# Performance work log

Hardware: AMD Instinct MI355X
Metric: run time of the kernel (lower is better)

The kernel has to match this reference:

```python
import jax, jax.numpy as jnp
import numpy as np

HEADS = 8
DIM_HEAD = 64
ROPE_THETA = 10000.0


def _rope(t):
    # t: [b, h, n, d]; interleaved-pair rotation as in rotary-embedding-torch
    n, d = t.shape[-2], t.shape[-1]
    inv_freq = 1.0 / (ROPE_THETA ** (jnp.arange(0, d, 2, dtype=jnp.float32) / d))  # [d/2]
    freqs = jnp.arange(n, dtype=jnp.float32)[:, None] * inv_freq[None, :]  # [n, d/2]
    freqs = jnp.repeat(freqs, 2, axis=-1)  # [n, d], repeated per pair
    cos, sin = jnp.cos(freqs), jnp.sin(freqs)
    x1 = t[..., 0::2]
    x2 = t[..., 1::2]
    rot = jnp.stack((-x2, x1), axis=-1).reshape(t.shape)  # rotate_half
    return t * cos + rot * sin


def setup_inputs() -> dict:
    key = jax.random.key(0)
    k1, k2, k3, k4 = jax.random.split(key, 4)
    b, n, dim = 2, 2048, 512
    hidden = HEADS * DIM_HEAD
    x = jax.random.normal(k1, (b, n, dim), dtype=jnp.float32)
    pos_bias = jax.random.normal(k2, (HEADS, n, n), dtype=jnp.float32) * 0.02
    w_qkv = jax.random.normal(k3, (dim, 3 * hidden), dtype=jnp.float32) * (dim ** -0.5)
    w_out = jax.random.normal(k4, (hidden, dim), dtype=jnp.float32) * (hidden ** -0.5)
    return {"x": x, "pos_bias": pos_bias, "w_qkv": w_qkv, "w_out": w_out}


def reference(x, pos_bias, w_qkv, w_out):
    b, n, _ = x.shape
    qkv = x @ w_qkv  # [b, n, 3*hidden]
    q, k, v = jnp.split(qkv, 3, axis=-1)

    def to_heads(t):
        return t.reshape(b, n, HEADS, DIM_HEAD).transpose(0, 2, 1, 3)  # [b,h,n,d]

    q, k, v = map(to_heads, (q, k, v))
    k = _rope(k)
    q = _rope(q * (DIM_HEAD ** -0.5))
    sim = jnp.einsum('bhid,bhjd->bhij', q, k)  # [b,h,n,n]
    sim = sim + pos_bias  # broadcast over batch
    sim = sim - jax.lax.stop_gradient(jnp.max(sim, axis=-1, keepdims=True))
    attn = jax.nn.softmax(sim, axis=-1)
    out = jnp.einsum('bhij,bhjd->bhid', attn, v)
    out = out.transpose(0, 2, 1, 3).reshape(b, n, HEADS * DIM_HEAD)
    return out @ w_out
```

## Files before the change

kernel.cpp:

```cpp
#include <hip/hip_runtime.h>
#include <math.h>

#define SEQ 2048
#define NHEAD 8
#define HDIM 64
#define BATCH 2

typedef __attribute__((ext_vector_type(8))) short short8;
typedef __attribute__((ext_vector_type(4))) float f32x4;

__device__ __forceinline__ ushort f2bf(float f) {
    union { float f; unsigned u; } v; v.f = f;
    unsigned r = v.u + 0x7FFFu + ((v.u >> 16) & 1u);
    return (ushort)(r >> 16);
}

__device__ __forceinline__ f32x4 mfma16(short8 a, short8 b, f32x4 c) {
    return __builtin_amdgcn_mfma_f32_16x16x32_bf16(a, b, c, 0, 0, 0);
}

__global__ __launch_bounds__(256)
void pack_x(const float* __restrict__ x, ushort* __restrict__ xb)
{
    const int i = (blockIdx.x * 256 + threadIdx.x) * 8;
    float4 a = *(const float4*)&x[i];
    float4 b = *(const float4*)&x[i + 4];
    union { ushort us[8]; uint4 v; } pk;
    pk.us[0] = f2bf(a.x); pk.us[1] = f2bf(a.y); pk.us[2] = f2bf(a.z); pk.us[3] = f2bf(a.w);
    pk.us[4] = f2bf(b.x); pk.us[5] = f2bf(b.y); pk.us[6] = f2bf(b.z); pk.us[7] = f2bf(b.w);
    *(uint4*)&xb[i] = pk.v;
}

__global__ __launch_bounds__(256)
void transpose_w(const float* __restrict__ w, ushort* __restrict__ wT, int K, int N)
{
    __shared__ ushort tile[64][66];
    const int t = threadIdx.x;
    const int n0 = blockIdx.x * 64, k0 = blockIdx.y * 64;
#pragma unroll
    for (int i = 0; i < 4; ++i) {
        const int slot = t + i * 256;
        const int r = slot >> 4, c4 = (slot & 15) * 4;
        float4 v = *(const float4*)&w[(size_t)(k0 + r) * N + n0 + c4];
        tile[c4 + 0][r] = f2bf(v.x);
        tile[c4 + 1][r] = f2bf(v.y);
        tile[c4 + 2][r] = f2bf(v.z);
        tile[c4 + 3][r] = f2bf(v.w);
    }
    __syncthreads();
    const int n = t >> 2, kc = (t & 3) * 16;
    union { ushort us[16]; uint4 v[2]; } o;
#pragma unroll
    for (int j = 0; j < 16; ++j) o.us[j] = tile[n][kc + j];
    *(uint4*)&wT[(size_t)(n0 + n) * K + k0 + kc]     = o.v[0];
    *(uint4*)&wT[(size_t)(n0 + n) * K + k0 + kc + 8] = o.v[1];
}

__global__ __launch_bounds__(256)
void gemm_qkv_rope(const ushort* __restrict__ xb, const ushort* __restrict__ wT,
                   ushort* __restrict__ qb, ushort* __restrict__ kb,
                   ushort* __restrict__ vtb)
{
    __shared__ __align__(16) ushort As[128][72];
    __shared__ __align__(16) ushort Bs[128][72];
    const int t = threadIdx.x, lane = t & 63, w = t >> 6;
    const int quad = lane >> 4, l16 = lane & 15;
    const int m0 = blockIdx.y * 128, n0 = blockIdx.x * 128;
    const int mw = (w >> 1) * 64, nw = (w & 1) * 64;
    f32x4 acc[4][4] = {};

    for (int k0 = 0; k0 < 512; k0 += 64) {
#pragma unroll
        for (int i = 0; i < 4; ++i) {
            const int slot = t + i * 256;
            const int r = slot >> 3, sg = (slot & 7) * 8;
            *(uint4*)&As[r][sg] = *(const uint4*)&xb[(size_t)(m0 + r) * 512 + k0 + sg];
            *(uint4*)&Bs[r][sg] = *(const uint4*)&wT[(size_t)(n0 + r) * 512 + k0 + sg];
        }
        __syncthreads();
#pragma unroll
        for (int ks = 0; ks < 2; ++ks) {
            short8 a[4], b[4];
#pragma unroll
            for (int i = 0; i < 4; ++i)
                a[i] = *(const short8*)&As[mw + i * 16 + l16][ks * 32 + quad * 8];
#pragma unroll
            for (int j = 0; j < 4; ++j)
                b[j] = *(const short8*)&Bs[nw + j * 16 + l16][ks * 32 + quad * 8];
#pragma unroll
            for (int i = 0; i < 4; ++i)
#pragma unroll
                for (int j = 0; j < 4; ++j)
                    acc[i][j] = mfma16(a[i], b[j], acc[i][j]);
        }
        __syncthreads();
    }

    const int sec = (n0 + nw) >> 9;
    if (sec == 2) {
#pragma unroll
        for (int i = 0; i < 4; ++i) {
            const int m = m0 + mw + i * 16 + quad * 4;
            const int bidx = m >> 11, n = m & 2047;
#pragma unroll
            for (int j = 0; j < 4; ++j) {
                const int nc = n0 + nw + j * 16 + l16;
                const int d = nc & 63, h = (nc >> 6) & 7;
                ushort4 pk;
                pk.x = f2bf(acc[i][j][0]); pk.y = f2bf(acc[i][j][1]);
                pk.z = f2bf(acc[i][j][2]); pk.w = f2bf(acc[i][j][3]);
                *(ushort4*)&vtb[(((size_t)bidx * 8 + h) * 64 + d) * 2048 + n] = pk;
            }
        }
    } else {
        ushort* dst = (sec == 0) ? qb : kb;
        const float scale = (sec == 0) ? 0.125f : 1.0f;
#pragma unroll
        for (int j = 0; j < 4; ++j) {
            const int nc = n0 + nw + j * 16 + l16;
            const int d = nc & 63, h = (nc >> 6) & 7;
            const float inv = __expf(-(float)(d & ~1) * (9.2103403719761836f / 64.0f));
#pragma unroll
            for (int i = 0; i < 4; ++i)
#pragma unroll
            for (int r = 0; r < 4; ++r) {
                const int m = m0 + mw + i * 16 + quad * 4 + r;
                const int bidx = m >> 11, n = m & 2047;
                float sn, cs;
                __sincosf((float)n * inv, &sn, &cs);
                const float vacc = acc[i][j][r];
                const float partner = __shfl_xor(vacc, 1);
                const float rot = (d & 1) ? (vacc * cs + partner * sn)
                                          : (vacc * cs - partner * sn);
                dst[(((size_t)bidx * 8 + h) * 2048 + n) * 64 + d] = f2bf(rot * scale);
            }
        }
    }
}

__global__ __launch_bounds__(256)
void flash_attn_mfma(const ushort* __restrict__ qb, const ushort* __restrict__ kb,
                     const ushort* __restrict__ vtb, const float* __restrict__ bias,
                     ushort* __restrict__ ob)
{
    __shared__ __align__(16) ushort Ks[64][72];
    __shared__ __align__(16) ushort Vt[64][72];
    __shared__ __align__(16) ushort Ps[4][16][72];
    const int t = threadIdx.x, lane = t & 63, w = t >> 6;
    const int quad = lane >> 4, l16 = lane & 15;
    const int q0 = blockIdx.x * 64, h = blockIdx.y, b = blockIdx.z;
    const size_t bh = (size_t)(b * NHEAD + h);
    const ushort* Q  = qb  + bh * SEQ * HDIM;
    const ushort* K  = kb  + bh * SEQ * HDIM;
    const ushort* VT = vtb + bh * HDIM * SEQ;

    short8 qf[2];
    qf[0] = *(const short8*)&Q[(size_t)(q0 + w * 16 + l16) * HDIM + quad * 8];
    qf[1] = *(const short8*)&Q[(size_t)(q0 + w * 16 + l16) * HDIM + 32 + quad * 8];

    f32x4 oacc[4] = {};
    float lsum[4] = {};
    const float* bias_base = bias + ((size_t)h * SEQ + q0 + w * 16 + quad * 4) * SEQ;

    for (int k0 = 0; k0 < SEQ; k0 += 64) {
        float bv[4][4];
#pragma unroll
        for (int r = 0; r < 4; ++r)
#pragma unroll
            for (int s = 0; s < 4; ++s)
                bv[r][s] = bias_base[(size_t)r * SEQ + k0 + s * 16 + l16];

#pragma unroll
        for (int i = 0; i < 2; ++i) {
            const int slot = t + i * 256;
            const int r = slot >> 3, sg = (slot & 7) * 8;
            *(uint4*)&Ks[r][sg] = *(const uint4*)&K[(size_t)(k0 + r) * HDIM + sg];
            *(uint4*)&Vt[r][sg] = *(const uint4*)&VT[(size_t)r * SEQ + k0 + sg];
        }
        __syncthreads();

        f32x4 sacc[4] = {};
#pragma unroll
        for (int ks = 0; ks < 2; ++ks)
#pragma unroll
            for (int s = 0; s < 4; ++s) {
                short8 kf = *(const short8*)&Ks[s * 16 + l16][ks * 32 + quad * 8];
                sacc[s] = mfma16(qf[ks], kf, sacc[s]);
            }

#pragma unroll
        for (int r = 0; r < 4; ++r) {
#pragma unroll
            for (int s = 0; s < 4; ++s) {
                const float p = __expf(sacc[s][r] + bv[r][s]);
                lsum[r] += p;
                Ps[w][quad * 4 + r][s * 16 + l16] = f2bf(p);
            }
        }
        asm volatile("" ::: "memory");

#pragma unroll
        for (int ks = 0; ks < 2; ++ks) {
            short8 pf = *(const short8*)&Ps[w][l16][ks * 32 + quad * 8];
#pragma unroll
            for (int s = 0; s < 4; ++s) {
                short8 vf = *(const short8*)&Vt[s * 16 + l16][ks * 32 + quad * 8];
                oacc[s] = mfma16(pf, vf, oacc[s]);
            }
        }
        __syncthreads();
    }

#pragma unroll
    for (int r = 0; r < 4; ++r) {
        float rs = lsum[r];
        rs += __shfl_xor(rs, 1, 16);
        rs += __shfl_xor(rs, 2, 16);
        rs += __shfl_xor(rs, 4, 16);
        rs += __shfl_xor(rs, 8, 16);
        const float invl = 1.0f / rs;
        const size_t m = (size_t)b * SEQ + q0 + w * 16 + quad * 4 + r;
#pragma unroll
        for (int s = 0; s < 4; ++s)
            ob[m * 512 + h * HDIM + s * 16 + l16] = f2bf(oacc[s][r] * invl);
    }
}

__global__ __launch_bounds__(256)
void gemm_out(const ushort* __restrict__ Ab, const ushort* __restrict__ wT,
              float* __restrict__ C)
{
    __shared__ __align__(16) ushort As[64][72];
    __shared__ __align__(16) ushort Bs[128][72];
    const int t = threadIdx.x, lane = t & 63, w = t >> 6;
    const int quad = lane >> 4, l16 = lane & 15;
    const int m0 = blockIdx.y * 64, n0 = blockIdx.x * 128;
    const int mw = (w >> 1) * 32, nw = (w & 1) * 64;
    f32x4 acc[2][4] = {};

    for (int k0 = 0; k0 < 512; k0 += 64) {
#pragma unroll
        for (int i = 0; i < 2; ++i) {
            const int slot = t + i * 256;
            const int r = slot >> 3, sg = (slot & 7) * 8;
            *(uint4*)&As[r][sg] = *(const uint4*)&Ab[(size_t)(m0 + r) * 512 + k0 + sg];
        }
#pragma unroll
        for (int i = 0; i < 4; ++i) {
            const int slot = t + i * 256;
            const int r = slot >> 3, sg = (slot & 7) * 8;
            *(uint4*)&Bs[r][sg] = *(const uint4*)&wT[(size_t)(n0 + r) * 512 + k0 + sg];
        }
        __syncthreads();
#pragma unroll
        for (int ks = 0; ks < 2; ++ks) {
            short8 a[2], b[4];
#pragma unroll
            for (int i = 0; i < 2; ++i)
                a[i] = *(const short8*)&As[mw + i * 16 + l16][ks * 32 + quad * 8];
#pragma unroll
            for (int j = 0; j < 4; ++j)
                b[j] = *(const short8*)&Bs[nw + j * 16 + l16][ks * 32 + quad * 8];
#pragma unroll
            for (int i = 0; i < 2; ++i)
#pragma unroll
                for (int j = 0; j < 4; ++j)
                    acc[i][j] = mfma16(a[i], b[j], acc[i][j]);
        }
        __syncthreads();
    }
#pragma unroll
    for (int i = 0; i < 2; ++i)
#pragma unroll
    for (int r = 0; r < 4; ++r) {
        const int m = m0 + mw + i * 16 + quad * 4 + r;
#pragma unroll
        for (int j = 0; j < 4; ++j)
            C[(size_t)m * 512 + n0 + nw + j * 16 + l16] = acc[i][j][r];
    }
}

extern "C" void kernel_launch(void* const* d_in, const int* in_sizes, int n_in,
                              void* d_out, int out_size, void* d_ws, size_t ws_size,
                              hipStream_t stream)
{
    const float* x        = (const float*)d_in[0];
    const float* pos_bias = (const float*)d_in[1];
    const float* w_qkv    = (const float*)d_in[2];
    const float* w_out    = (const float*)d_in[3];
    float* out = (float*)d_out;

    char* ws = (char*)d_ws;
    ushort* xb     = (ushort*)(ws);
    ushort* wqkvT  = (ushort*)(ws + 4194304);
    ushort* woutT  = (ushort*)(ws + 5767168);
    ushort* qb     = (ushort*)(ws + 6291456);
    ushort* kb     = (ushort*)(ws + 10485760);
    ushort* vtb    = (ushort*)(ws + 14680064);
    ushort* attnb  = (ushort*)(ws + 18874368);

    pack_x<<<1024, 256, 0, stream>>>(x, xb);
    transpose_w<<<dim3(24, 8), 256, 0, stream>>>(w_qkv, wqkvT, 512, 1536);
    transpose_w<<<dim3(8, 8), 256, 0, stream>>>(w_out, woutT, 512, 512);
    gemm_qkv_rope<<<dim3(12, 32), 256, 0, stream>>>(xb, wqkvT, qb, kb, vtb);
    flash_attn_mfma<<<dim3(SEQ / 64, NHEAD, BATCH), 256, 0, stream>>>(qb, kb, vtb, pos_bias, attnb);
    gemm_out<<<dim3(4, 64), 256, 0, stream>>>(attnb, woutT, out);
}
```

Measured before the change: 285.3 us.

## Split attention over key chunks, prefetch tiles, merge prep kernels, shrink GEMM tiles

Merges the x-pack and the two weight transposes into one launch. The attention kernel is split four ways along the key axis, with a new combine kernel that sums the partial outputs and row sums, which raises the grid from 512 to 2048 blocks. K, V and bias tiles are now register-prefetched one step ahead, and the two GEMMs use smaller tiles with register prefetch to get more blocks per GPU. The split adds fp32 partial-output traffic through workspace and an extra launch. Combining partials without any max rescaling is still exact, because the original kernel also did not subtract a running max.

```diff
diff --git a/kernel.cpp b/kernel.cpp
--- a/kernel.cpp
+++ b/kernel.cpp
@@ -20,23 +20,25 @@
 }
 
 __global__ __launch_bounds__(256)
-void pack_x(const float* __restrict__ x, ushort* __restrict__ xb)
-{
-    const int i = (blockIdx.x * 256 + threadIdx.x) * 8;
-    float4 a = *(const float4*)&x[i];
-    float4 b = *(const float4*)&x[i + 4];
-    union { ushort us[8]; uint4 v; } pk;
-    pk.us[0] = f2bf(a.x); pk.us[1] = f2bf(a.y); pk.us[2] = f2bf(a.z); pk.us[3] = f2bf(a.w);
-    pk.us[4] = f2bf(b.x); pk.us[5] = f2bf(b.y); pk.us[6] = f2bf(b.z); pk.us[7] = f2bf(b.w);
-    *(uint4*)&xb[i] = pk.v;
-}
-
-__global__ __launch_bounds__(256)
-void transpose_w(const float* __restrict__ w, ushort* __restrict__ wT, int K, int N)
+void prep(const float* __restrict__ x, const float* __restrict__ w_qkv,
+          const float* __restrict__ w_out, ushort* __restrict__ xb,
+          ushort* __restrict__ wqkvT, ushort* __restrict__ woutT)
 {
     __shared__ ushort tile[64][66];
-    const int t = threadIdx.x;
-    const int n0 = blockIdx.x * 64, k0 = blockIdx.y * 64;
+    const int blk = blockIdx.x, t = threadIdx.x;
+    if (blk < 1024) {
+        const int i = (blk * 256 + t) * 8;
+        float4 a = *(const float4*)&x[i];
+        float4 b = *(const float4*)&x[i + 4];
+        union { ushort us[8]; uint4 v; } pk;
+        pk.us[0] = f2bf(a.x); pk.us[1] = f2bf(a.y); pk.us[2] = f2bf(a.z); pk.us[3] = f2bf(a.w);
+        pk.us[4] = f2bf(b.x); pk.us[5] = f2bf(b.y); pk.us[6] = f2bf(b.z); pk.us[7] = f2bf(b.w);
+        *(uint4*)&xb[i] = pk.v;
+        return;
+    }
+    const float* w; ushort* wT; int K, N, n0, k0;
+    if (blk < 1216) { const int s = blk - 1024; w = w_qkv; wT = wqkvT; K = 512; N = 1536; n0 = (s % 24) * 64; k0 = (s / 24) * 64; }
+    else            { const int s = blk - 1216; w = w_out; wT = woutT; K = 512; N = 512;  n0 = (s % 8) * 64;  k0 = (s / 8) * 64; }
 #pragma unroll
     for (int i = 0; i < 4; ++i) {
         const int slot = t + i * 256;
@@ -61,34 +63,48 @@
                    ushort* __restrict__ qb, ushort* __restrict__ kb,
                    ushort* __restrict__ vtb)
 {
-    __shared__ __align__(16) ushort As[128][72];
+    __shared__ __align__(16) ushort As[64][72];
     __shared__ __align__(16) ushort Bs[128][72];
     const int t = threadIdx.x, lane = t & 63, w = t >> 6;
     const int quad = lane >> 4, l16 = lane & 15;
-    const int m0 = blockIdx.y * 128, n0 = blockIdx.x * 128;
-    const int mw = (w >> 1) * 64, nw = (w & 1) * 64;
-    f32x4 acc[4][4] = {};
+    const int m0 = blockIdx.y * 64, n0 = blockIdx.x * 128;
+    const int mw = (w >> 1) * 32, nw = (w & 1) * 64;
+    f32x4 acc[2][4] = {};
+
+    const int ra = t >> 3, sg = (t & 7) * 8;
+    uint4 ar[2], br[4];
+#pragma unroll
+    for (int i = 0; i < 2; ++i)
+        ar[i] = *(const uint4*)&xb[(size_t)(m0 + ra + i * 32) * 512 + sg];
+#pragma unroll
+    for (int i = 0; i < 4; ++i)
+        br[i] = *(const uint4*)&wT[(size_t)(n0 + ra + i * 32) * 512 + sg];
 
     for (int k0 = 0; k0 < 512; k0 += 64) {
 #pragma unroll
-        for (int i = 0; i < 4; ++i) {
-            const int slot = t + i * 256;
-            const int r = slot >> 3, sg = (slot & 7) * 8;
-            *(uint4*)&As[r][sg] = *(const uint4*)&xb[(size_t)(m0 + r) * 512 + k0 + sg];
-            *(uint4*)&Bs[r][sg] = *(const uint4*)&wT[(size_t)(n0 + r) * 512 + k0 + sg];
-        }
-        __syncthreads();
+        for (int i = 0; i < 2; ++i) *(uint4*)&As[ra + i * 32][sg] = ar[i];
+#pragma unroll
+        for (int i = 0; i < 4; ++i) *(uint4*)&Bs[ra + i * 32][sg] = br[i];
+        __syncthreads();
+        if (k0 < 448) {
+#pragma unroll
+            for (int i = 0; i < 2; ++i)
+                ar[i] = *(const uint4*)&xb[(size_t)(m0 + ra + i * 32) * 512 + k0 + 64 + sg];
+#pragma unroll
+            for (int i = 0; i < 4; ++i)
+                br[i] = *(const uint4*)&wT[(size_t)(n0 + ra + i * 32) * 512 + k0 + 64 + sg];
+        }
 #pragma unroll
         for (int ks = 0; ks < 2; ++ks) {
-            short8 a[4], b[4];
-#pragma unroll
-            for (int i = 0; i < 4; ++i)
+            short8 a[2], b[4];
+#pragma unroll
+            for (int i = 0; i < 2; ++i)
                 a[i] = *(const short8*)&As[mw + i * 16 + l16][ks * 32 + quad * 8];
 #pragma unroll
             for (int j = 0; j < 4; ++j)
                 b[j] = *(const short8*)&Bs[nw + j * 16 + l16][ks * 32 + quad * 8];
 #pragma unroll
-            for (int i = 0; i < 4; ++i)
+            for (int i = 0; i < 2; ++i)
 #pragma unroll
                 for (int j = 0; j < 4; ++j)
                     acc[i][j] = mfma16(a[i], b[j], acc[i][j]);
@@ -99,7 +115,7 @@
     const int sec = (n0 + nw) >> 9;
     if (sec == 2) {
 #pragma unroll
-        for (int i = 0; i < 4; ++i) {
+        for (int i = 0; i < 2; ++i) {
             const int m = m0 + mw + i * 16 + quad * 4;
             const int bidx = m >> 11, n = m & 2047;
 #pragma unroll
@@ -121,7 +137,7 @@
             const int d = nc & 63, h = (nc >> 6) & 7;
             const float inv = __expf(-(float)(d & ~1) * (9.2103403719761836f / 64.0f));
 #pragma unroll
-            for (int i = 0; i < 4; ++i)
+            for (int i = 0; i < 2; ++i)
 #pragma unroll
             for (int r = 0; r < 4; ++r) {
                 const int m = m0 + mw + i * 16 + quad * 4 + r;
@@ -139,16 +155,18 @@
 }
 
 __global__ __launch_bounds__(256)
-void flash_attn_mfma(const ushort* __restrict__ qb, const ushort* __restrict__ kb,
-                     const ushort* __restrict__ vtb, const float* __restrict__ bias,
-                     ushort* __restrict__ ob)
+void flash_attn_split(const ushort* __restrict__ qb, const ushort* __restrict__ kb,
+                      const ushort* __restrict__ vtb, const float* __restrict__ bias,
+                      float* __restrict__ opart, float* __restrict__ lsump)
 {
     __shared__ __align__(16) ushort Ks[64][72];
     __shared__ __align__(16) ushort Vt[64][72];
     __shared__ __align__(16) ushort Ps[4][16][72];
     const int t = threadIdx.x, lane = t & 63, w = t >> 6;
     const int quad = lane >> 4, l16 = lane & 15;
-    const int q0 = blockIdx.x * 64, h = blockIdx.y, b = blockIdx.z;
+    const int q0 = blockIdx.x * 64, h = blockIdx.y;
+    const int b = blockIdx.z >> 2, split = blockIdx.z & 3;
+    const int kbase = split * 512;
     const size_t bh = (size_t)(b * NHEAD + h);
     const ushort* Q  = qb  + bh * SEQ * HDIM;
     const ushort* K  = kb  + bh * SEQ * HDIM;
@@ -162,22 +180,43 @@
     float lsum[4] = {};
     const float* bias_base = bias + ((size_t)h * SEQ + q0 + w * 16 + quad * 4) * SEQ;
 
-    for (int k0 = 0; k0 < SEQ; k0 += 64) {
-        float bv[4][4];
-#pragma unroll
-        for (int r = 0; r < 4; ++r)
-#pragma unroll
-            for (int s = 0; s < 4; ++s)
-                bv[r][s] = bias_base[(size_t)r * SEQ + k0 + s * 16 + l16];
-
+    const int ra = t >> 3, sg = (t & 7) * 8;
+    uint4 kr[2], vr[2];
+#pragma unroll
+    for (int i = 0; i < 2; ++i) {
+        kr[i] = *(const uint4*)&K[(size_t)(kbase + ra + i * 32) * HDIM + sg];
+        vr[i] = *(const uint4*)&VT[(size_t)(ra + i * 32) * SEQ + kbase + sg];
+    }
+    float bv[4][4];
+#pragma unroll
+    for (int r = 0; r < 4; ++r)
+#pragma unroll
+        for (int s = 0; s < 4; ++s)
+            bv[r][s] = bias_base[(size_t)r * SEQ + kbase + s * 16 + l16];
+
+#pragma unroll
+    for (int it = 0; it < 8; ++it) {
+        const int k0 = kbase + it * 64;
 #pragma unroll
         for (int i = 0; i < 2; ++i) {
-            const int slot = t + i * 256;
-            const int r = slot >> 3, sg = (slot & 7) * 8;
-            *(uint4*)&Ks[r][sg] = *(const uint4*)&K[(size_t)(k0 + r) * HDIM + sg];
-            *(uint4*)&Vt[r][sg] = *(const uint4*)&VT[(size_t)r * SEQ + k0 + sg];
-        }
-        __syncthreads();
+            *(uint4*)&Ks[ra + i * 32][sg] = kr[i];
+            *(uint4*)&Vt[ra + i * 32][sg] = vr[i];
+        }
+        __syncthreads();
+
+        float bvn[4][4];
+        if (it < 7) {
+#pragma unroll
+            for (int i = 0; i < 2; ++i) {
+                kr[i] = *(const uint4*)&K[(size_t)(k0 + 64 + ra + i * 32) * HDIM + sg];
+                vr[i] = *(const uint4*)&VT[(size_t)(ra + i * 32) * SEQ + k0 + 64 + sg];
+            }
+#pragma unroll
+            for (int r = 0; r < 4; ++r)
+#pragma unroll
+                for (int s = 0; s < 4; ++s)
+                    bvn[r][s] = bias_base[(size_t)r * SEQ + k0 + 64 + s * 16 + l16];
+        }
 
         f32x4 sacc[4] = {};
 #pragma unroll
@@ -189,14 +228,13 @@
             }
 
 #pragma unroll
-        for (int r = 0; r < 4; ++r) {
+        for (int r = 0; r < 4; ++r)
 #pragma unroll
             for (int s = 0; s < 4; ++s) {
                 const float p = __expf(sacc[s][r] + bv[r][s]);
                 lsum[r] += p;
                 Ps[w][quad * 4 + r][s * 16 + l16] = f2bf(p);
             }
-        }
         asm volatile("" ::: "memory");
 
 #pragma unroll
@@ -209,21 +247,53 @@
             }
         }
         __syncthreads();
-    }
-
+
+        if (it < 7) {
+#pragma unroll
+            for (int r = 0; r < 4; ++r)
+#pragma unroll
+                for (int s = 0; s < 4; ++s) bv[r][s] = bvn[r][s];
+        }
+    }
+
+    const size_t pbase = ((size_t)bh * 4 + split) * SEQ;
 #pragma unroll
     for (int r = 0; r < 4; ++r) {
+        const int row = q0 + w * 16 + quad * 4 + r;
         float rs = lsum[r];
         rs += __shfl_xor(rs, 1, 16);
         rs += __shfl_xor(rs, 2, 16);
         rs += __shfl_xor(rs, 4, 16);
         rs += __shfl_xor(rs, 8, 16);
-        const float invl = 1.0f / rs;
-        const size_t m = (size_t)b * SEQ + q0 + w * 16 + quad * 4 + r;
 #pragma unroll
         for (int s = 0; s < 4; ++s)
-            ob[m * 512 + h * HDIM + s * 16 + l16] = f2bf(oacc[s][r] * invl);
-    }
+            opart[(pbase + row) * 64 + s * 16 + l16] = oacc[s][r];
+        if (l16 == 0) lsump[pbase + row] = rs;
+    }
+}
+
+__global__ __launch_bounds__(256)
+void combine(const float* __restrict__ opart, const float* __restrict__ lsump,
+             ushort* __restrict__ attnb)
+{
+    const int tid = blockIdx.x * 256 + threadIdx.x;
+    const int d4 = (tid & 15) * 4;
+    const int n  = (tid >> 4) & 2047;
+    const int bh = tid >> 15;
+    float ox = 0, oy = 0, oz = 0, ow = 0, L = 0;
+#pragma unroll
+    for (int s = 0; s < 4; ++s) {
+        const size_t base = ((size_t)bh * 4 + s) * SEQ + n;
+        float4 p = *(const float4*)&opart[base * 64 + d4];
+        ox += p.x; oy += p.y; oz += p.z; ow += p.w;
+        L += lsump[base];
+    }
+    const float inv = 1.0f / L;
+    ushort4 pk;
+    pk.x = f2bf(ox * inv); pk.y = f2bf(oy * inv);
+    pk.z = f2bf(oz * inv); pk.w = f2bf(ow * inv);
+    const int b = bh >> 3, h = bh & 7;
+    *(ushort4*)&attnb[((size_t)b * SEQ + n) * 512 + h * 64 + d4] = pk;
 }
 
 __global__ __launch_bounds__(256)
@@ -231,40 +301,48 @@
               float* __restrict__ C)
 {
     __shared__ __align__(16) ushort As[64][72];
-    __shared__ __align__(16) ushort Bs[128][72];
+    __shared__ __align__(16) ushort Bs[64][72];
     const int t = threadIdx.x, lane = t & 63, w = t >> 6;
     const int quad = lane >> 4, l16 = lane & 15;
-    const int m0 = blockIdx.y * 64, n0 = blockIdx.x * 128;
-    const int mw = (w >> 1) * 32, nw = (w & 1) * 64;
-    f32x4 acc[2][4] = {};
+    const int m0 = blockIdx.y * 64, n0 = blockIdx.x * 64;
+    const int mw = (w >> 1) * 32, nw = (w & 1) * 32;
+    f32x4 acc[2][2] = {};
+
+    const int ra = t >> 3, sg = (t & 7) * 8;
+    uint4 ar[2], br[2];
+#pragma unroll
+    for (int i = 0; i < 2; ++i) {
+        ar[i] = *(const uint4*)&Ab[(size_t)(m0 + ra + i * 32) * 512 + sg];
+        br[i] = *(const uint4*)&wT[(size_t)(n0 + ra + i * 32) * 512 + sg];
+    }
 
     for (int k0 = 0; k0 < 512; k0 += 64) {
 #pragma unroll
         for (int i = 0; i < 2; ++i) {
-            const int slot = t + i * 256;
-            const int r = slot >> 3, sg = (slot & 7) * 8;
-            *(uint4*)&As[r][sg] = *(const uint4*)&Ab[(size_t)(m0 + r) * 512 + k0 + sg];
-        }
-#pragma unroll
-        for (int i = 0; i < 4; ++i) {
-            const int slot = t + i * 256;
-            const int r = slot >> 3, sg = (slot & 7) * 8;
-            *(uint4*)&Bs[r][sg] = *(const uint4*)&wT[(size_t)(n0 + r) * 512 + k0 + sg];
-        }
-        __syncthreads();
+            *(uint4*)&As[ra + i * 32][sg] = ar[i];
+            *(uint4*)&Bs[ra + i * 32][sg] = br[i];
+        }
+        __syncthreads();
+        if (k0 < 448) {
+#pragma unroll
+            for (int i = 0; i < 2; ++i) {
+                ar[i] = *(const uint4*)&Ab[(size_t)(m0 + ra + i * 32) * 512 + k0 + 64 + sg];
+                br[i] = *(const uint4*)&wT[(size_t)(n0 + ra + i * 32) * 512 + k0 + 64 + sg];
+            }
+        }
 #pragma unroll
         for (int ks = 0; ks < 2; ++ks) {
-            short8 a[2], b[4];
+            short8 a[2], b[2];
 #pragma unroll
             for (int i = 0; i < 2; ++i)
                 a[i] = *(const short8*)&As[mw + i * 16 + l16][ks * 32 + quad * 8];
 #pragma unroll
-            for (int j = 0; j < 4; ++j)
+            for (int j = 0; j < 2; ++j)
                 b[j] = *(const short8*)&Bs[nw + j * 16 + l16][ks * 32 + quad * 8];
 #pragma unroll
             for (int i = 0; i < 2; ++i)
 #pragma unroll
-                for (int j = 0; j < 4; ++j)
+                for (int j = 0; j < 2; ++j)
                     acc[i][j] = mfma16(a[i], b[j], acc[i][j]);
         }
         __syncthreads();
@@ -275,7 +353,7 @@
     for (int r = 0; r < 4; ++r) {
         const int m = m0 + mw + i * 16 + quad * 4 + r;
 #pragma unroll
-        for (int j = 0; j < 4; ++j)
+        for (int j = 0; j < 2; ++j)
             C[(size_t)m * 512 + n0 + nw + j * 16 + l16] = acc[i][j][r];
     }
 }
@@ -298,11 +376,12 @@
     ushort* kb     = (ushort*)(ws + 10485760);
     ushort* vtb    = (ushort*)(ws + 14680064);
     ushort* attnb  = (ushort*)(ws + 18874368);
-
-    pack_x<<<1024, 256, 0, stream>>>(x, xb);
-    transpose_w<<<dim3(24, 8), 256, 0, stream>>>(w_qkv, wqkvT, 512, 1536);
-    transpose_w<<<dim3(8, 8), 256, 0, stream>>>(w_out, woutT, 512, 512);
-    gemm_qkv_rope<<<dim3(12, 32), 256, 0, stream>>>(xb, wqkvT, qb, kb, vtb);
-    flash_attn_mfma<<<dim3(SEQ / 64, NHEAD, BATCH), 256, 0, stream>>>(qb, kb, vtb, pos_bias, attnb);
-    gemm_out<<<dim3(4, 64), 256, 0, stream>>>(attnb, woutT, out);
-}
+    float*  opart  = (float*) (ws + 23068672);
+    float*  lsump  = (float*) (ws + 56623104);
+
+    prep<<<1280, 256, 0, stream>>>(x, w_qkv, w_out, xb, wqkvT, woutT);
+    gemm_qkv_rope<<<dim3(12, 64), 256, 0, stream>>>(xb, wqkvT, qb, kb, vtb);
+    flash_attn_split<<<dim3(SEQ / 64, NHEAD, BATCH * 4), 256, 0, stream>>>(qb, kb, vtb, pos_bias, opart, lsump);
+    combine<<<2048, 256, 0, stream>>>(opart, lsump, attnb);
+    gemm_out<<<dim3(8, 64), 256, 0, stream>>>(attnb, woutT, out);
+}
```

After: 353.8 us. 24.0% more time.

## Merge prep kernels and switch GEMMs and attention to single-wave register-fed blocks

Applied to the files above, without the earlier changes.

Folds the three preprocessing kernels into one launch. Rewrites both GEMMs and the attention kernel as one-wavefront blocks that load MFMA operands straight from global memory instead of staging them through shared memory with block barriers. Attention now double-buffers K, V and bias fragments in registers to overlap loads with compute. This removes LDS traffic and syncs, at the cost of losing operand reuse across waves (more global/L2 traffic) and higher register pressure.

```diff
diff --git a/kernel.cpp b/kernel.cpp
--- a/kernel.cpp
+++ b/kernel.cpp
@@ -20,23 +20,25 @@
 }
 
 __global__ __launch_bounds__(256)
-void pack_x(const float* __restrict__ x, ushort* __restrict__ xb)
-{
-    const int i = (blockIdx.x * 256 + threadIdx.x) * 8;
-    float4 a = *(const float4*)&x[i];
-    float4 b = *(const float4*)&x[i + 4];
-    union { ushort us[8]; uint4 v; } pk;
-    pk.us[0] = f2bf(a.x); pk.us[1] = f2bf(a.y); pk.us[2] = f2bf(a.z); pk.us[3] = f2bf(a.w);
-    pk.us[4] = f2bf(b.x); pk.us[5] = f2bf(b.y); pk.us[6] = f2bf(b.z); pk.us[7] = f2bf(b.w);
-    *(uint4*)&xb[i] = pk.v;
-}
-
-__global__ __launch_bounds__(256)
-void transpose_w(const float* __restrict__ w, ushort* __restrict__ wT, int K, int N)
+void prep(const float* __restrict__ x, const float* __restrict__ w_qkv,
+          const float* __restrict__ w_out, ushort* __restrict__ xb,
+          ushort* __restrict__ wqkvT, ushort* __restrict__ woutT)
 {
     __shared__ ushort tile[64][66];
-    const int t = threadIdx.x;
-    const int n0 = blockIdx.x * 64, k0 = blockIdx.y * 64;
+    const int blk = blockIdx.x, t = threadIdx.x;
+    if (blk < 1024) {
+        const int i = (blk * 256 + t) * 8;
+        float4 a = *(const float4*)&x[i];
+        float4 b = *(const float4*)&x[i + 4];
+        union { ushort us[8]; uint4 v; } pk;
+        pk.us[0] = f2bf(a.x); pk.us[1] = f2bf(a.y); pk.us[2] = f2bf(a.z); pk.us[3] = f2bf(a.w);
+        pk.us[4] = f2bf(b.x); pk.us[5] = f2bf(b.y); pk.us[6] = f2bf(b.z); pk.us[7] = f2bf(b.w);
+        *(uint4*)&xb[i] = pk.v;
+        return;
+    }
+    const float* w; ushort* wT; int K, N, n0, k0;
+    if (blk < 1216) { const int s = blk - 1024; w = w_qkv; wT = wqkvT; K = 512; N = 1536; n0 = (s % 24) * 64; k0 = (s / 24) * 64; }
+    else            { const int s = blk - 1216; w = w_out; wT = woutT; K = 512; N = 512;  n0 = (s % 8) * 64;  k0 = (s / 8) * 64; }
 #pragma unroll
     for (int i = 0; i < 4; ++i) {
         const int slot = t + i * 256;
@@ -56,56 +58,40 @@
     *(uint4*)&wT[(size_t)(n0 + n) * K + k0 + kc + 8] = o.v[1];
 }
 
-__global__ __launch_bounds__(256)
+__global__ __launch_bounds__(64)
 void gemm_qkv_rope(const ushort* __restrict__ xb, const ushort* __restrict__ wT,
                    ushort* __restrict__ qb, ushort* __restrict__ kb,
                    ushort* __restrict__ vtb)
 {
-    __shared__ __align__(16) ushort As[128][72];
-    __shared__ __align__(16) ushort Bs[128][72];
-    const int t = threadIdx.x, lane = t & 63, w = t >> 6;
-    const int quad = lane >> 4, l16 = lane & 15;
-    const int m0 = blockIdx.y * 128, n0 = blockIdx.x * 128;
-    const int mw = (w >> 1) * 64, nw = (w & 1) * 64;
-    f32x4 acc[4][4] = {};
-
-    for (int k0 = 0; k0 < 512; k0 += 64) {
-#pragma unroll
-        for (int i = 0; i < 4; ++i) {
-            const int slot = t + i * 256;
-            const int r = slot >> 3, sg = (slot & 7) * 8;
-            *(uint4*)&As[r][sg] = *(const uint4*)&xb[(size_t)(m0 + r) * 512 + k0 + sg];
-            *(uint4*)&Bs[r][sg] = *(const uint4*)&wT[(size_t)(n0 + r) * 512 + k0 + sg];
-        }
-        __syncthreads();
-#pragma unroll
-        for (int ks = 0; ks < 2; ++ks) {
-            short8 a[4], b[4];
-#pragma unroll
-            for (int i = 0; i < 4; ++i)
-                a[i] = *(const short8*)&As[mw + i * 16 + l16][ks * 32 + quad * 8];
+    const int lane = threadIdx.x, quad = lane >> 4, l16 = lane & 15;
+    const int n0 = blockIdx.x * 64, m0 = blockIdx.y * 32;
+    f32x4 acc[2][4] = {};
+
+#pragma unroll 4
+    for (int k0 = 0; k0 < 512; k0 += 32) {
+        short8 a[2], bfr[4];
+#pragma unroll
+        for (int i = 0; i < 2; ++i)
+            a[i] = *(const short8*)&xb[(size_t)(m0 + i * 16 + l16) * 512 + k0 + quad * 8];
+#pragma unroll
+        for (int j = 0; j < 4; ++j)
+            bfr[j] = *(const short8*)&wT[(size_t)(n0 + j * 16 + l16) * 512 + k0 + quad * 8];
+#pragma unroll
+        for (int i = 0; i < 2; ++i)
 #pragma unroll
             for (int j = 0; j < 4; ++j)
-                b[j] = *(const short8*)&Bs[nw + j * 16 + l16][ks * 32 + quad * 8];
-#pragma unroll
-            for (int i = 0; i < 4; ++i)
-#pragma unroll
-                for (int j = 0; j < 4; ++j)
-                    acc[i][j] = mfma16(a[i], b[j], acc[i][j]);
-        }
-        __syncthreads();
-    }
-
-    const int sec = (n0 + nw) >> 9;
+                acc[i][j] = mfma16(a[i], bfr[j], acc[i][j]);
+    }
+
+    const int sec = n0 >> 9;
     if (sec == 2) {
 #pragma unroll
-        for (int i = 0; i < 4; ++i) {
-            const int m = m0 + mw + i * 16 + quad * 4;
+        for (int i = 0; i < 2; ++i) {
+            const int m = m0 + i * 16 + quad * 4;
             const int bidx = m >> 11, n = m & 2047;
 #pragma unroll
             for (int j = 0; j < 4; ++j) {
-                const int nc = n0 + nw + j * 16 + l16;
-                const int d = nc & 63, h = (nc >> 6) & 7;
+                const int d = j * 16 + l16, h = (n0 >> 6) & 7;
                 ushort4 pk;
                 pk.x = f2bf(acc[i][j][0]); pk.y = f2bf(acc[i][j][1]);
                 pk.z = f2bf(acc[i][j][2]); pk.w = f2bf(acc[i][j][3]);
@@ -117,14 +103,13 @@
         const float scale = (sec == 0) ? 0.125f : 1.0f;
 #pragma unroll
         for (int j = 0; j < 4; ++j) {
-            const int nc = n0 + nw + j * 16 + l16;
-            const int d = nc & 63, h = (nc >> 6) & 7;
+            const int d = j * 16 + l16, h = (n0 >> 6) & 7;
             const float inv = __expf(-(float)(d & ~1) * (9.2103403719761836f / 64.0f));
 #pragma unroll
-            for (int i = 0; i < 4; ++i)
+            for (int i = 0; i < 2; ++i)
 #pragma unroll
             for (int r = 0; r < 4; ++r) {
-                const int m = m0 + mw + i * 16 + quad * 4 + r;
+                const int m = m0 + i * 16 + quad * 4 + r;
                 const int bidx = m >> 11, n = m & 2047;
                 float sn, cs;
                 __sincosf((float)n * inv, &sn, &cs);
@@ -138,77 +123,86 @@
     }
 }
 
-__global__ __launch_bounds__(256)
-void flash_attn_mfma(const ushort* __restrict__ qb, const ushort* __restrict__ kb,
+__global__ __launch_bounds__(64)
+void flash_attn_wave(const ushort* __restrict__ qb, const ushort* __restrict__ kb,
                      const ushort* __restrict__ vtb, const float* __restrict__ bias,
                      ushort* __restrict__ ob)
 {
-    __shared__ __align__(16) ushort Ks[64][72];
-    __shared__ __align__(16) ushort Vt[64][72];
-    __shared__ __align__(16) ushort Ps[4][16][72];
-    const int t = threadIdx.x, lane = t & 63, w = t >> 6;
-    const int quad = lane >> 4, l16 = lane & 15;
-    const int q0 = blockIdx.x * 64, h = blockIdx.y, b = blockIdx.z;
+    __shared__ __align__(16) ushort Ps[16][72];
+    const int lane = threadIdx.x, quad = lane >> 4, l16 = lane & 15;
+    const int q0 = blockIdx.x * 16, h = blockIdx.y, b = blockIdx.z;
     const size_t bh = (size_t)(b * NHEAD + h);
     const ushort* Q  = qb  + bh * SEQ * HDIM;
-    const ushort* K  = kb  + bh * SEQ * HDIM;
+    const ushort* Kp = kb  + bh * SEQ * HDIM;
     const ushort* VT = vtb + bh * HDIM * SEQ;
 
     short8 qf[2];
-    qf[0] = *(const short8*)&Q[(size_t)(q0 + w * 16 + l16) * HDIM + quad * 8];
-    qf[1] = *(const short8*)&Q[(size_t)(q0 + w * 16 + l16) * HDIM + 32 + quad * 8];
+    qf[0] = *(const short8*)&Q[(size_t)(q0 + l16) * HDIM + quad * 8];
+    qf[1] = *(const short8*)&Q[(size_t)(q0 + l16) * HDIM + 32 + quad * 8];
 
     f32x4 oacc[4] = {};
     float lsum[4] = {};
-    const float* bias_base = bias + ((size_t)h * SEQ + q0 + w * 16 + quad * 4) * SEQ;
-
-    for (int k0 = 0; k0 < SEQ; k0 += 64) {
-        float bv[4][4];
+    const float* bias_base = bias + ((size_t)h * SEQ + q0 + quad * 4) * SEQ;
+
+    short8 kf[2][2][4], vf[2][2][4];
+    float bv[2][4][4];
+#pragma unroll
+    for (int ks = 0; ks < 2; ++ks)
+#pragma unroll
+        for (int s = 0; s < 4; ++s) {
+            kf[0][ks][s] = *(const short8*)&Kp[(size_t)(s * 16 + l16) * HDIM + ks * 32 + quad * 8];
+            vf[0][ks][s] = *(const short8*)&VT[(size_t)(s * 16 + l16) * SEQ + ks * 32 + quad * 8];
+        }
+#pragma unroll
+    for (int r = 0; r < 4; ++r)
+#pragma unroll
+        for (int s = 0; s < 4; ++s)
+            bv[0][r][s] = bias_base[(size_t)r * SEQ + s * 16 + l16];
+
+#pragma unroll 2
+    for (int it = 0; it < 32; ++it) {
+        const int cur = it & 1, nxt = cur ^ 1;
+        const int k0 = it * 64;
+
+        if (it < 31) {
+#pragma unroll
+            for (int ks = 0; ks < 2; ++ks)
+#pragma unroll
+                for (int s = 0; s < 4; ++s) {
+                    kf[nxt][ks][s] = *(const short8*)&Kp[(size_t)(k0 + 64 + s * 16 + l16) * HDIM + ks * 32 + quad * 8];
+                    vf[nxt][ks][s] = *(const short8*)&VT[(size_t)(s * 16 + l16) * SEQ + k0 + 64 + ks * 32 + quad * 8];
+                }
+#pragma unroll
+            for (int r = 0; r < 4; ++r)
+#pragma unroll
+                for (int s = 0; s < 4; ++s)
+                    bv[nxt][r][s] = bias_base[(size_t)r * SEQ + k0 + 64 + s * 16 + l16];
+        }
+
+        f32x4 sacc[4] = {};
+#pragma unroll
+        for (int ks = 0; ks < 2; ++ks)
+#pragma unroll
+            for (int s = 0; s < 4; ++s)
+                sacc[s] = mfma16(qf[ks], kf[cur][ks][s], sacc[s]);
+
 #pragma unroll
         for (int r = 0; r < 4; ++r)
 #pragma unroll
+            for (int s = 0; s < 4; ++s) {
+                const float p = __expf(sacc[s][r] + bv[cur][r][s]);
+                lsum[r] += p;
+                Ps[quad * 4 + r][s * 16 + l16] = f2bf(p);
+            }
+        asm volatile("" ::: "memory");
+
+#pragma unroll
+        for (int ks = 0; ks < 2; ++ks) {
+            short8 pf = *(const short8*)&Ps[l16][ks * 32 + quad * 8];
+#pragma unroll
             for (int s = 0; s < 4; ++s)
-                bv[r][s] = bias_base[(size_t)r * SEQ + k0 + s * 16 + l16];
-
-#pragma unroll
-        for (int i = 0; i < 2; ++i) {
-            const int slot = t + i * 256;
-            const int r = slot >> 3, sg = (slot & 7) * 8;
-            *(uint4*)&Ks[r][sg] = *(const uint4*)&K[(size_t)(k0 + r) * HDIM + sg];
-            *(uint4*)&Vt[r][sg] = *(const uint4*)&VT[(size_t)r * SEQ + k0 + sg];
-        }
-        __syncthreads();
-
-        f32x4 sacc[4] = {};
-#pragma unroll
-        for (int ks = 0; ks < 2; ++ks)
-#pragma unroll
-            for (int s = 0; s < 4; ++s) {
-                short8 kf = *(const short8*)&Ks[s * 16 + l16][ks * 32 + quad * 8];
-                sacc[s] = mfma16(qf[ks], kf, sacc[s]);
-            }
-
-#pragma unroll
-        for (int r = 0; r < 4; ++r) {
-#pragma unroll
-            for (int s = 0; s < 4; ++s) {
-                const float p = __expf(sacc[s][r] + bv[r][s]);
-                lsum[r] += p;
-                Ps[w][quad * 4 + r][s * 16 + l16] = f2bf(p);
-            }
-        }
-        asm volatile("" ::: "memory");
-
-#pragma unroll
-        for (int ks = 0; ks < 2; ++ks) {
-            short8 pf = *(const short8*)&Ps[w][l16][ks * 32 + quad * 8];
-#pragma unroll
-            for (int s = 0; s < 4; ++s) {
-                short8 vf = *(const short8*)&Vt[s * 16 + l16][ks * 32 + quad * 8];
-                oacc[s] = mfma16(pf, vf, oacc[s]);
-            }
-        }
-        __syncthreads();
+                oacc[s] = mfma16(pf, vf[cur][ks][s], oacc[s]);
+        }
     }
 
 #pragma unroll
@@ -219,64 +213,44 @@
         rs += __shfl_xor(rs, 4, 16);
         rs += __shfl_xor(rs, 8, 16);
         const float invl = 1.0f / rs;
-        const size_t m = (size_t)b * SEQ + q0 + w * 16 + quad * 4 + r;
+        const size_t m = (size_t)b * SEQ + q0 + quad * 4 + r;
 #pragma unroll
         for (int s = 0; s < 4; ++s)
             ob[m * 512 + h * HDIM + s * 16 + l16] = f2bf(oacc[s][r] * invl);
     }
 }
 
-__global__ __launch_bounds__(256)
+__global__ __launch_bounds__(64)
 void gemm_out(const ushort* __restrict__ Ab, const ushort* __restrict__ wT,
               float* __restrict__ C)
 {
-    __shared__ __align__(16) ushort As[64][72];
-    __shared__ __align__(16) ushort Bs[128][72];
-    const int t = threadIdx.x, lane = t & 63, w = t >> 6;
-    const int quad = lane >> 4, l16 = lane & 15;
-    const int m0 = blockIdx.y * 64, n0 = blockIdx.x * 128;
-    const int mw = (w >> 1) * 32, nw = (w & 1) * 64;
+    const int lane = threadIdx.x, quad = lane >> 4, l16 = lane & 15;
+    const int n0 = blockIdx.x * 64, m0 = blockIdx.y * 32;
     f32x4 acc[2][4] = {};
 
-    for (int k0 = 0; k0 < 512; k0 += 64) {
-#pragma unroll
-        for (int i = 0; i < 2; ++i) {
-            const int slot = t + i * 256;
-            const int r = slot >> 3, sg = (slot & 7) * 8;
-            *(uint4*)&As[r][sg] = *(const uint4*)&Ab[(size_t)(m0 + r) * 512 + k0 + sg];
-        }
-#pragma unroll
-        for (int i = 0; i < 4; ++i) {
-            const int slot = t + i * 256;
-            const int r = slot >> 3, sg = (slot & 7) * 8;
-            *(uint4*)&Bs[r][sg] = *(const uint4*)&wT[(size_t)(n0 + r) * 512 + k0 + sg];
-        }
-        __syncthreads();
-#pragma unroll
-        for (int ks = 0; ks < 2; ++ks) {
-            short8 a[2], b[4];
-#pragma unroll
-            for (int i = 0; i < 2; ++i)
-                a[i] = *(const short8*)&As[mw + i * 16 + l16][ks * 32 + quad * 8];
+#pragma unroll 4
+    for (int k0 = 0; k0 < 512; k0 += 32) {
+        short8 a[2], bfr[4];
+#pragma unroll
+        for (int i = 0; i < 2; ++i)
+            a[i] = *(const short8*)&Ab[(size_t)(m0 + i * 16 + l16) * 512 + k0 + quad * 8];
+#pragma unroll
+        for (int j = 0; j < 4; ++j)
+            bfr[j] = *(const short8*)&wT[(size_t)(n0 + j * 16 + l16) * 512 + k0 + quad * 8];
+#pragma unroll
+        for (int i = 0; i < 2; ++i)
 #pragma unroll
             for (int j = 0; j < 4; ++j)
-                b[j] = *(const short8*)&Bs[nw + j * 16 + l16][ks * 32 + quad * 8];
-#pragma unroll
-            for (int i = 0; i < 2; ++i)
-#pragma unroll
-                for (int j = 0; j < 4; ++j)
-                    acc[i][j] = mfma16(a[i], b[j], acc[i][j]);
-        }
-        __syncthreads();
+                acc[i][j] = mfma16(a[i], bfr[j], acc[i][j]);
     }
 #pragma unroll
     for (int i = 0; i < 2; ++i)
 #pragma unroll
     for (int r = 0; r < 4; ++r) {
-        const int m = m0 + mw + i * 16 + quad * 4 + r;
+        const int m = m0 + i * 16 + quad * 4 + r;
 #pragma unroll
         for (int j = 0; j < 4; ++j)
-            C[(size_t)m * 512 + n0 + nw + j * 16 + l16] = acc[i][j][r];
+            C[(size_t)m * 512 + n0 + j * 16 + l16] = acc[i][j][r];
     }
 }
 
@@ -299,10 +273,8 @@
     ushort* vtb    = (ushort*)(ws + 14680064);
     ushort* attnb  = (ushort*)(ws + 18874368);
 
-    pack_x<<<1024, 256, 0, stream>>>(x, xb);
-    transpose_w<<<dim3(24, 8), 256, 0, stream>>>(w_qkv, wqkvT, 512, 1536);
-    transpose_w<<<dim3(8, 8), 256, 0, stream>>>(w_out, woutT, 512, 512);
-    gemm_qkv_rope<<<dim3(12, 32), 256, 0, stream>>>(xb, wqkvT, qb, kb, vtb);
-    flash_attn_mfma<<<dim3(SEQ / 64, NHEAD, BATCH), 256, 0, stream>>>(qb, kb, vtb, pos_bias, attnb);
-    gemm_out<<<dim3(4, 64), 256, 0, stream>>>(attnb, woutT, out);
-}
+    prep<<<1280, 256, 0, stream>>>(x, w_qkv, w_out, xb, wqkvT, woutT);
+    gemm_qkv_rope<<<dim3(24, 128), 64, 0, stream>>>(xb, wqkvT, qb, kb, vtb);
+    flash_attn_wave<<<dim3(SEQ / 16, NHEAD, BATCH), 64, 0, stream>>>(qb, kb, vtb, pos_bias, attnb);
+    gemm_out<<<dim3(8, 128), 64, 0, stream>>>(attnb, woutT, out);
+}
```

New measurement: 356.8 us. 1.25x slower.

## Use direct global-to-LDS loads, merge prep kernels, shrink GEMM tiles

Applied to the files above, without the earlier changes.

Merges the x packing and both weight transposes into one prep launch. The QKV, attention and output kernels now fill shared memory with global_load_lds 16-byte transfers instead of register round trips, and the LDS row padding is dropped to fit that layout. The attention kernel also stages the fp32 position-bias tile through LDS. The GEMM tiles are halved to launch more blocks. The unpadded LDS rows risk bank conflicts on the MFMA fragment reads, and the trailing barrier is moved to the top of each iteration.

```diff
diff --git a/kernel.cpp b/kernel.cpp
--- a/kernel.cpp
+++ b/kernel.cpp
@@ -19,24 +19,32 @@
     return __builtin_amdgcn_mfma_f32_16x16x32_bf16(a, b, c, 0, 0, 0);
 }
 
+__device__ __forceinline__ void gld16(const void* g, void* l) {
+    __builtin_amdgcn_global_load_lds(
+        (const __attribute__((address_space(1))) unsigned int*)g,
+        (__attribute__((address_space(3))) unsigned int*)l, 16, 0, 0);
+}
+
 __global__ __launch_bounds__(256)
-void pack_x(const float* __restrict__ x, ushort* __restrict__ xb)
-{
-    const int i = (blockIdx.x * 256 + threadIdx.x) * 8;
-    float4 a = *(const float4*)&x[i];
-    float4 b = *(const float4*)&x[i + 4];
-    union { ushort us[8]; uint4 v; } pk;
-    pk.us[0] = f2bf(a.x); pk.us[1] = f2bf(a.y); pk.us[2] = f2bf(a.z); pk.us[3] = f2bf(a.w);
-    pk.us[4] = f2bf(b.x); pk.us[5] = f2bf(b.y); pk.us[6] = f2bf(b.z); pk.us[7] = f2bf(b.w);
-    *(uint4*)&xb[i] = pk.v;
-}
-
-__global__ __launch_bounds__(256)
-void transpose_w(const float* __restrict__ w, ushort* __restrict__ wT, int K, int N)
+void prep(const float* __restrict__ x, const float* __restrict__ w_qkv,
+          const float* __restrict__ w_out, ushort* __restrict__ xb,
+          ushort* __restrict__ wqkvT, ushort* __restrict__ woutT)
 {
     __shared__ ushort tile[64][66];
-    const int t = threadIdx.x;
-    const int n0 = blockIdx.x * 64, k0 = blockIdx.y * 64;
+    const int blk = blockIdx.x, t = threadIdx.x;
+    if (blk < 1024) {
+        const int i = (blk * 256 + t) * 8;
+        float4 a = *(const float4*)&x[i];
+        float4 b = *(const float4*)&x[i + 4];
+        union { ushort us[8]; uint4 v; } pk;
+        pk.us[0] = f2bf(a.x); pk.us[1] = f2bf(a.y); pk.us[2] = f2bf(a.z); pk.us[3] = f2bf(a.w);
+        pk.us[4] = f2bf(b.x); pk.us[5] = f2bf(b.y); pk.us[6] = f2bf(b.z); pk.us[7] = f2bf(b.w);
+        *(uint4*)&xb[i] = pk.v;
+        return;
+    }
+    const float* w; ushort* wT; int K, N, n0, k0;
+    if (blk < 1216) { const int s = blk - 1024; w = w_qkv; wT = wqkvT; K = 512; N = 1536; n0 = (s % 24) * 64; k0 = (s / 24) * 64; }
+    else            { const int s = blk - 1216; w = w_out; wT = woutT; K = 512; N = 512;  n0 = (s % 8) * 64;  k0 = (s / 8) * 64; }
 #pragma unroll
     for (int i = 0; i < 4; ++i) {
         const int slot = t + i * 256;
@@ -61,45 +69,46 @@
                    ushort* __restrict__ qb, ushort* __restrict__ kb,
                    ushort* __restrict__ vtb)
 {
-    __shared__ __align__(16) ushort As[128][72];
-    __shared__ __align__(16) ushort Bs[128][72];
+    __shared__ __align__(16) ushort As[64][64];
+    __shared__ __align__(16) ushort Bs[128][64];
     const int t = threadIdx.x, lane = t & 63, w = t >> 6;
     const int quad = lane >> 4, l16 = lane & 15;
-    const int m0 = blockIdx.y * 128, n0 = blockIdx.x * 128;
-    const int mw = (w >> 1) * 64, nw = (w & 1) * 64;
-    f32x4 acc[4][4] = {};
+    const int m0 = blockIdx.y * 64, n0 = blockIdx.x * 128;
+    const int mw = (w >> 1) * 32, nw = (w & 1) * 64;
+    const int krow = lane >> 3, kcol = (lane & 7) * 8;
+    f32x4 acc[2][4] = {};
 
     for (int k0 = 0; k0 < 512; k0 += 64) {
-#pragma unroll
-        for (int i = 0; i < 4; ++i) {
-            const int slot = t + i * 256;
-            const int r = slot >> 3, sg = (slot & 7) * 8;
-            *(uint4*)&As[r][sg] = *(const uint4*)&xb[(size_t)(m0 + r) * 512 + k0 + sg];
-            *(uint4*)&Bs[r][sg] = *(const uint4*)&wT[(size_t)(n0 + r) * 512 + k0 + sg];
+        __syncthreads();
+        gld16(&xb[(size_t)(m0 + w * 8 + krow) * 512 + k0 + kcol],        &As[w * 8][0]);
+        gld16(&xb[(size_t)(m0 + (w + 4) * 8 + krow) * 512 + k0 + kcol],  &As[(w + 4) * 8][0]);
+#pragma unroll
+        for (int jj = 0; jj < 4; ++jj) {
+            const int j = w * 4 + jj;
+            gld16(&wT[(size_t)(n0 + j * 8 + krow) * 512 + k0 + kcol], &Bs[j * 8][0]);
         }
         __syncthreads();
 #pragma unroll
         for (int ks = 0; ks < 2; ++ks) {
-            short8 a[4], b[4];
-#pragma unroll
-            for (int i = 0; i < 4; ++i)
+            short8 a[2], b[4];
+#pragma unroll
+            for (int i = 0; i < 2; ++i)
                 a[i] = *(const short8*)&As[mw + i * 16 + l16][ks * 32 + quad * 8];
 #pragma unroll
             for (int j = 0; j < 4; ++j)
                 b[j] = *(const short8*)&Bs[nw + j * 16 + l16][ks * 32 + quad * 8];
 #pragma unroll
-            for (int i = 0; i < 4; ++i)
+            for (int i = 0; i < 2; ++i)
 #pragma unroll
                 for (int j = 0; j < 4; ++j)
                     acc[i][j] = mfma16(a[i], b[j], acc[i][j]);
         }
-        __syncthreads();
     }
 
     const int sec = (n0 + nw) >> 9;
     if (sec == 2) {
 #pragma unroll
-        for (int i = 0; i < 4; ++i) {
+        for (int i = 0; i < 2; ++i) {
             const int m = m0 + mw + i * 16 + quad * 4;
             const int bidx = m >> 11, n = m & 2047;
 #pragma unroll
@@ -121,7 +130,7 @@
             const int d = nc & 63, h = (nc >> 6) & 7;
             const float inv = __expf(-(float)(d & ~1) * (9.2103403719761836f / 64.0f));
 #pragma unroll
-            for (int i = 0; i < 4; ++i)
+            for (int i = 0; i < 2; ++i)
 #pragma unroll
             for (int r = 0; r < 4; ++r) {
                 const int m = m0 + mw + i * 16 + quad * 4 + r;
@@ -143,15 +152,16 @@
                      const ushort* __restrict__ vtb, const float* __restrict__ bias,
                      ushort* __restrict__ ob)
 {
-    __shared__ __align__(16) ushort Ks[64][72];
-    __shared__ __align__(16) ushort Vt[64][72];
+    __shared__ __align__(16) ushort Ks[64][64];
+    __shared__ __align__(16) ushort Vt[64][64];
+    __shared__ __align__(16) float  Bl[64][64];
     __shared__ __align__(16) ushort Ps[4][16][72];
     const int t = threadIdx.x, lane = t & 63, w = t >> 6;
     const int quad = lane >> 4, l16 = lane & 15;
     const int q0 = blockIdx.x * 64, h = blockIdx.y, b = blockIdx.z;
     const size_t bh = (size_t)(b * NHEAD + h);
     const ushort* Q  = qb  + bh * SEQ * HDIM;
-    const ushort* K  = kb  + bh * SEQ * HDIM;
+    const ushort* Kp = kb  + bh * SEQ * HDIM;
     const ushort* VT = vtb + bh * HDIM * SEQ;
 
     short8 qf[2];
@@ -160,22 +170,20 @@
 
     f32x4 oacc[4] = {};
     float lsum[4] = {};
-    const float* bias_base = bias + ((size_t)h * SEQ + q0 + w * 16 + quad * 4) * SEQ;
-
-    for (int k0 = 0; k0 < SEQ; k0 += 64) {
-        float bv[4][4];
-#pragma unroll
-        for (int r = 0; r < 4; ++r)
-#pragma unroll
-            for (int s = 0; s < 4; ++s)
-                bv[r][s] = bias_base[(size_t)r * SEQ + k0 + s * 16 + l16];
-
-#pragma unroll
-        for (int i = 0; i < 2; ++i) {
-            const int slot = t + i * 256;
-            const int r = slot >> 3, sg = (slot & 7) * 8;
-            *(uint4*)&Ks[r][sg] = *(const uint4*)&K[(size_t)(k0 + r) * HDIM + sg];
-            *(uint4*)&Vt[r][sg] = *(const uint4*)&VT[(size_t)r * SEQ + k0 + sg];
+    const int krow = lane >> 3, kcol = (lane & 7) * 8;
+    const int brow = lane >> 4, bcol = (lane & 15) * 4;
+
+    for (int it = 0; it < 32; ++it) {
+        const int k0 = it * 64;
+        __syncthreads();
+        gld16(&Kp[(size_t)(k0 + w * 8 + krow) * HDIM + kcol],       &Ks[w * 8][0]);
+        gld16(&Kp[(size_t)(k0 + (w + 4) * 8 + krow) * HDIM + kcol], &Ks[(w + 4) * 8][0]);
+        gld16(&VT[(size_t)(w * 8 + krow) * SEQ + k0 + kcol],        &Vt[w * 8][0]);
+        gld16(&VT[(size_t)((w + 4) * 8 + krow) * SEQ + k0 + kcol],  &Vt[(w + 4) * 8][0]);
+#pragma unroll
+        for (int jj = 0; jj < 4; ++jj) {
+            const int j = w * 4 + jj;
+            gld16(&bias[((size_t)h * SEQ + q0 + j * 4 + brow) * SEQ + k0 + bcol], &Bl[j * 4][0]);
         }
         __syncthreads();
 
@@ -189,14 +197,13 @@
             }
 
 #pragma unroll
-        for (int r = 0; r < 4; ++r) {
+        for (int r = 0; r < 4; ++r)
 #pragma unroll
             for (int s = 0; s < 4; ++s) {
-                const float p = __expf(sacc[s][r] + bv[r][s]);
+                const float p = __expf(sacc[s][r] + Bl[w * 16 + quad * 4 + r][s * 16 + l16]);
                 lsum[r] += p;
                 Ps[w][quad * 4 + r][s * 16 + l16] = f2bf(p);
             }
-        }
         asm volatile("" ::: "memory");
 
 #pragma unroll
@@ -208,7 +215,6 @@
                 oacc[s] = mfma16(pf, vf, oacc[s]);
             }
         }
-        __syncthreads();
     }
 
 #pragma unroll
@@ -230,44 +236,37 @@
 void gemm_out(const ushort* __restrict__ Ab, const ushort* __restrict__ wT,
               float* __restrict__ C)
 {
-    __shared__ __align__(16) ushort As[64][72];
-    __shared__ __align__(16) ushort Bs[128][72];
+    __shared__ __align__(16) ushort As[64][64];
+    __shared__ __align__(16) ushort Bs[64][64];
     const int t = threadIdx.x, lane = t & 63, w = t >> 6;
     const int quad = lane >> 4, l16 = lane & 15;
-    const int m0 = blockIdx.y * 64, n0 = blockIdx.x * 128;
-    const int mw = (w >> 1) * 32, nw = (w & 1) * 64;
-    f32x4 acc[2][4] = {};
+    const int m0 = blockIdx.y * 64, n0 = blockIdx.x * 64;
+    const int mw = (w >> 1) * 32, nw = (w & 1) * 32;
+    const int krow = lane >> 3, kcol = (lane & 7) * 8;
+    f32x4 acc[2][2] = {};
 
     for (int k0 = 0; k0 < 512; k0 += 64) {
-#pragma unroll
-        for (int i = 0; i < 2; ++i) {
-            const int slot = t + i * 256;
-            const int r = slot >> 3, sg = (slot & 7) * 8;
-            *(uint4*)&As[r][sg] = *(const uint4*)&Ab[(size_t)(m0 + r) * 512 + k0 + sg];
-        }
-#pragma unroll
-        for (int i = 0; i < 4; ++i) {
-            const int slot = t + i * 256;
-            const int r = slot >> 3, sg = (slot & 7) * 8;
-            *(uint4*)&Bs[r][sg] = *(const uint4*)&wT[(size_t)(n0 + r) * 512 + k0 + sg];
-        }
+        __syncthreads();
+        gld16(&Ab[(size_t)(m0 + w * 8 + krow) * 512 + k0 + kcol],       &As[w * 8][0]);
+        gld16(&Ab[(size_t)(m0 + (w + 4) * 8 + krow) * 512 + k0 + kcol], &As[(w + 4) * 8][0]);
+        gld16(&wT[(size_t)(n0 + w * 8 + krow) * 512 + k0 + kcol],       &Bs[w * 8][0]);
+        gld16(&wT[(size_t)(n0 + (w + 4) * 8 + krow) * 512 + k0 + kcol], &Bs[(w + 4) * 8][0]);
         __syncthreads();
 #pragma unroll
         for (int ks = 0; ks < 2; ++ks) {
-            short8 a[2], b[4];
+            short8 a[2], b[2];
 #pragma unroll
             for (int i = 0; i < 2; ++i)
                 a[i] = *(const short8*)&As[mw + i * 16 + l16][ks * 32 + quad * 8];
 #pragma unroll
-            for (int j = 0; j < 4; ++j)
+            for (int j = 0; j < 2; ++j)
                 b[j] = *(const short8*)&Bs[nw + j * 16 + l16][ks * 32 + quad * 8];
 #pragma unroll
             for (int i = 0; i < 2; ++i)
 #pragma unroll
-                for (int j = 0; j < 4; ++j)
+                for (int j = 0; j < 2; ++j)
                     acc[i][j] = mfma16(a[i], b[j], acc[i][j]);
         }
-        __syncthreads();
     }
 #pragma unroll
     for (int i = 0; i < 2; ++i)
@@ -275,7 +274,7 @@
     for (int r = 0; r < 4; ++r) {
         const int m = m0 + mw + i * 16 + quad * 4 + r;
 #pragma unroll
-        for (int j = 0; j < 4; ++j)
+        for (int j = 0; j < 2; ++j)
             C[(size_t)m * 512 + n0 + nw + j * 16 + l16] = acc[i][j][r];
     }
 }
@@ -299,10 +298,8 @@
     ushort* vtb    = (ushort*)(ws + 14680064);
     ushort* attnb  = (ushort*)(ws + 18874368);
 
-    pack_x<<<1024, 256, 0, stream>>>(x, xb);
-    transpose_w<<<dim3(24, 8), 256, 0, stream>>>(w_qkv, wqkvT, 512, 1536);
-    transpose_w<<<dim3(8, 8), 256, 0, stream>>>(w_out, woutT, 512, 512);
-    gemm_qkv_rope<<<dim3(12, 32), 256, 0, stream>>>(xb, wqkvT, qb, kb, vtb);
+    prep<<<1280, 256, 0, stream>>>(x, w_qkv, w_out, xb, wqkvT, woutT);
+    gemm_qkv_rope<<<dim3(12, 64), 256, 0, stream>>>(xb, wqkvT, qb, kb, vtb);
     flash_attn_mfma<<<dim3(SEQ / 64, NHEAD, BATCH), 256, 0, stream>>>(qb, kb, vtb, pos_bias, attnb);
-    gemm_out<<<dim3(4, 64), 256, 0, stream>>>(attnb, woutT, out);
-}
+    gemm_out<<<dim3(8, 64), 256, 0, stream>>>(attnb, woutT, out);
+}
```

Measured after the change: 257.2 us. 9.8% less time.
